# Optimization experiments

Hardware: AMD Instinct MI355X
Metric: run time of the kernel (lower is better)

Reference implementation:

```python
import jax, jax.numpy as jnp
import numpy as np

B, T, S = 64, 128, 16
E = 512           # d2v input size
H = 512           # bi-LSTM output size (args.d2v_embed)
Hh = H // 2       # per-direction hidden
NL = 2            # num_layers
ED = 128          # args.embedding_dim
USERS, ARTS, PAD = 100000, 100000, 0


def setup_inputs() -> dict:
    key = jax.random.key(0)
    ks = jax.random.split(key, 32)
    p = 0.02
    inp = {}
    inp["x1"] = jax.random.normal(ks[0], (B, T, E), jnp.float32)
    inp["sample_d2v_embeds"] = jax.random.normal(ks[1], (B, T, S, H), jnp.float32)
    # LSTM params: layer-0 input E == layer-1 input H, so stackable. gate order i,f,g,o
    inp["lstm_Wih"] = jax.random.normal(ks[2], (NL, 2, 4 * Hh, E), jnp.float32) * p
    inp["lstm_Whh"] = jax.random.normal(ks[3], (NL, 2, 4 * Hh, Hh), jnp.float32) * p
    inp["lstm_bih"] = jax.random.normal(ks[4], (NL, 2, 4 * Hh), jnp.float32) * p
    inp["lstm_bhh"] = jax.random.normal(ks[5], (NL, 2, 4 * Hh), jnp.float32) * p
    inp["attn_W1"] = jax.random.normal(ks[6], (H, H), jnp.float32) * p
    inp["attn_b1"] = jax.random.normal(ks[7], (H,), jnp.float32) * p
    inp["attn_w2"] = jax.random.normal(ks[8], (H,), jnp.float32) * p
    inp["rnn_mlp_W"] = jax.random.normal(ks[9], (64, H), jnp.float32) * p
    inp["rnn_mlp_b"] = jax.random.normal(ks[10], (64,), jnp.float32) * p
    inp["user_table"] = jax.random.normal(ks[11], (USERS, ED), jnp.float32) * p
    inp["art_table"] = (jax.random.normal(ks[12], (ARTS, ED), jnp.float32) * p).at[PAD].set(0.0)
    inp["em_W1"] = jax.random.normal(ks[13], (128, ED), jnp.float32) * p
    inp["em_b1"] = jax.random.normal(ks[14], (128,), jnp.float32) * p
    inp["em_W2"] = jax.random.normal(ks[15], (64, 128), jnp.float32) * p
    inp["em_b2"] = jax.random.normal(ks[16], (64,), jnp.float32) * p
    inp["lm_W1"] = jax.random.normal(ks[17], (256, 128), jnp.float32) * p
    inp["lm_b1"] = jax.random.normal(ks[18], (256,), jnp.float32) * p
    inp["lm_W2"] = jax.random.normal(ks[19], (128, 256), jnp.float32) * p
    inp["lm_b2"] = jax.random.normal(ks[20], (128,), jnp.float32) * p
    inp["lm_W3"] = jax.random.normal(ks[21], (64, 128), jnp.float32) * p
    inp["lm_b3"] = jax.random.normal(ks[22], (64,), jnp.float32) * p
    inp["lm_W4"] = jax.random.normal(ks[23], (1, 64), jnp.float32) * p
    inp["lm_b4"] = jax.random.normal(ks[24], (1,), jnp.float32) * p
    inp["x2"] = 0  # unused '_' arg
    inp["cate"] = jax.random.randint(ks[25], (B, T), 0, 10)  # unused by forward
    lens = jax.random.randint(ks[26], (B,), 1, T + 1)
    inp["seq_lens"] = jnp.sort(lens)[::-1]  # pack requires descending
    inp["user_ids"] = jax.random.randint(ks[27], (B,), 0, USERS)
    inp["sample_ids"] = jax.random.randint(ks[28], (B, T, S), 0, ARTS)
    return inp


def _bilstm(x, lens, Wih, Whh, bih, bhh):
    # Packed bidirectional LSTM == padded LSTM with state updates masked to t < len.
    Bc, Tc, _ = x.shape
    tmask = jnp.arange(Tc)[None, :] < lens[:, None]       # [B,T]
    m_t = tmask.T[:, :, None]                             # [T,B,1]
    for l in range(NL):
        outs = []
        for d, rev in ((0, False), (1, True)):
            xg = jnp.einsum('bti,gi->tbg', x, Wih[l, d]) + bih[l, d]  # [T,B,4Hh]
            Whh_ld, bhh_ld = Whh[l, d], bhh[l, d]

            def step(carry, inp_t, Whh_ld=Whh_ld, bhh_ld=bhh_ld):
                h, c = carry
                xg_t, m = inp_t
                g = xg_t + h @ Whh_ld.T + bhh_ld
                i_, f_, g_, o_ = jnp.split(g, 4, axis=-1)
                c2 = jax.nn.sigmoid(f_) * c + jax.nn.sigmoid(i_) * jnp.tanh(g_)
                h2 = jax.nn.sigmoid(o_) * jnp.tanh(c2)
                h = jnp.where(m, h2, h)
                c = jnp.where(m, c2, c)
                return (h, c), h

            init = (jnp.zeros((Bc, Hh), x.dtype), jnp.zeros((Bc, Hh), x.dtype))
            _, hs = jax.lax.scan(step, init, (xg, m_t), reverse=rev)
            outs.append(jnp.transpose(hs, (1, 0, 2)))
        x = jnp.concatenate(outs, axis=-1)                # [B,T,H]
    return x, tmask


def reference(x1, sample_d2v_embeds, lstm_Wih, lstm_Whh, lstm_bih, lstm_bhh,
              attn_W1, attn_b1, attn_w2, rnn_mlp_W, rnn_mlp_b,
              user_table, art_table, em_W1, em_b1, em_W2, em_b2,
              lm_W1, lm_b1, lm_W2, lm_b2, lm_W3, lm_b3, lm_W4, lm_b4,
              x2, cate, seq_lens, user_ids, sample_ids):
    rnn, tmask = _bilstm(x1, seq_lens, lstm_Wih, lstm_Whh, lstm_bih, lstm_bhh)
    # per-key MLP attention score, causal softmax, weighted sum (the packed double loop)
    sc = jnp.einsum('bth,h->bt', jnp.tanh(jnp.einsum('bth,oh->bto', rnn, attn_W1) + attn_b1), attn_w2)
    causal = jnp.tril(jnp.ones((rnn.shape[1], rnn.shape[1]), bool))
    logits = jnp.where(causal[None, :, :], sc[:, None, :], jnp.float32(-1e30))
    a = jax.nn.softmax(logits, axis=-1)                   # [B,T(query),T(key)]
    ctx = jnp.einsum('bts,bsh->bth', a, rnn)
    ctx = jnp.where(tmask[:, :, None], ctx, 0.0)          # rnn_step zeros at padded t
    # embedding branch
    ue = user_table[user_ids]                             # [B,ED]
    se = art_table[sample_ids]                            # [B,T,S,ED]
    e = ue[:, None, None, :] * se
    e = jax.nn.relu(e @ em_W1.T + em_b1)
    e = jax.nn.relu(e @ em_W2.T + em_b2)                  # [B,T,S,64]
    # rnn branch
    r = ctx[:, :, None, :] * sample_d2v_embeds
    r = r @ rnn_mlp_W.T + rnn_mlp_b                       # [B,T,S,64]
    z = jnp.concatenate([e, r], axis=-1)                  # [B,T,S,128]
    z = jax.nn.relu(z @ lm_W1.T + lm_b1)
    z = jax.nn.relu(z @ lm_W2.T + lm_b2)
    z = jax.nn.relu(z @ lm_W3.T + lm_b3)
    z = jax.nn.sigmoid(z @ lm_W4.T + lm_b4)
    return jnp.squeeze(z, axis=-1)                        # [B,T,S]
```

## Files before the change

kernel.cpp:

```cpp
#include <hip/hip_runtime.h>
#include <cstddef>

namespace {

constexpr int T = 128;

typedef unsigned short u16;
typedef unsigned int u32;
typedef __attribute__((ext_vector_type(8))) short short8;
typedef __attribute__((ext_vector_type(4))) float f32x4;
typedef __attribute__((ext_vector_type(4))) int i32x4;

__device__ __forceinline__ u16 f2bf(float x) {
  u32 u = __float_as_uint(x);
  u = (u + 0x7FFFu + ((u >> 16) & 1u)) >> 16;
  return (u16)u;
}
__device__ __forceinline__ float bf2f(u16 v) {
  return __uint_as_float(((u32)v) << 16);
}
__device__ __forceinline__ float sigf(float x) {
  return __builtin_amdgcn_rcpf(1.f + __builtin_amdgcn_exp2f(-1.44269504f * x));
}
__device__ __forceinline__ float tanh2(float x) {
  return 1.f - 2.f * __builtin_amdgcn_rcpf(1.f + __builtin_amdgcn_exp2f(2.88539008f * x));
}
__device__ __forceinline__ void bar_lds() {
  asm volatile("s_waitcnt lgkmcnt(0)\n\ts_barrier" ::: "memory");
}

constexpr int O_WIH = 0;
constexpr int O_AW1 = 2097152;
constexpr int O_EM1 = 2359296;
constexpr int O_EM2 = 2375680;
constexpr int O_MLP = 2383872;
constexpr int O_LW1 = 2416640;
constexpr int O_LW2 = 2449408;
constexpr int O_LW3 = 2482176;
constexpr int N_WBF = 2490368;

__global__ __launch_bounds__(256)
void k_prep(const float* __restrict__ wih, const float* __restrict__ aw1,
            const float* __restrict__ e1, const float* __restrict__ e2,
            const float* __restrict__ mw, const float* __restrict__ l1,
            const float* __restrict__ l2, const float* __restrict__ l3,
            u16* __restrict__ wbf) {
  int i = blockIdx.x * 256 + threadIdx.x;
  if (i >= N_WBF) return;
  float v;
  if (i < O_AW1)      v = wih[i];
  else if (i < O_EM1) v = aw1[i - O_AW1];
  else if (i < O_EM2) v = e1[i - O_EM1];
  else if (i < O_MLP) v = e2[i - O_EM2];
  else if (i < O_LW1) v = mw[i - O_MLP];
  else if (i < O_LW2) v = l1[i - O_LW1];
  else if (i < O_LW3) v = l2[i - O_LW2];
  else                v = l3[i - O_LW3];
  wbf[i] = f2bf(v);
}

__global__ __launch_bounds__(256)
void k_prepw(const float* __restrict__ whh, signed char* __restrict__ wq) {
  int i = blockIdx.x * 256 + threadIdx.x;
  float v = whh[i] * 1016.f;
  v = fminf(fmaxf(v, -127.f), 127.f);
  wq[i] = (signed char)(int)rintf(v);
}

__global__ __launch_bounds__(256)
void k_xg_mfma(const float* __restrict__ X, const u16* __restrict__ Wbf,
               const float* __restrict__ bi, const float* __restrict__ bh,
               float* __restrict__ xg) {
  __shared__ __align__(16) u16 sx[32 * 520];
  int tid = threadIdx.x;
  int rowbase = blockIdx.x * 32;
  int nchunk = blockIdx.y;
  for (int idx = tid; idx < 4096; idx += 256) {
    int r = idx >> 7, k4 = idx & 127;
    float4 v = *(const float4*)(X + (size_t)(rowbase + r) * 512 + k4 * 4);
    u32* p = (u32*)(sx + r * 520 + k4 * 4);
    p[0] = (u32)f2bf(v.x) | ((u32)f2bf(v.y) << 16);
    p[1] = (u32)f2bf(v.z) | ((u32)f2bf(v.w) << 16);
  }
  __syncthreads();
  int w = tid >> 6, lane = tid & 63;
  int msub = w >> 1, nhalf = w & 1;
  int mbase = msub * 16;
  int nb0 = nchunk * 256 + nhalf * 128;
  f32x4 acc[8];
#pragma unroll
  for (int i = 0; i < 8; ++i) acc[i] = f32x4{0.f, 0.f, 0.f, 0.f};
  for (int kt = 0; kt < 16; ++kt) {
    short8 a = *(const short8*)(sx + (mbase + (lane & 15)) * 520 + kt * 32 + (lane >> 4) * 8);
#pragma unroll
    for (int nt = 0; nt < 8; ++nt) {
      short8 b = *(const short8*)(Wbf + (size_t)(nb0 + nt * 16 + (lane & 15)) * 512 +
                                  kt * 32 + (lane >> 4) * 8);
      acc[nt] = __builtin_amdgcn_mfma_f32_16x16x32_bf16(a, b, acc[nt], 0, 0, 0);
    }
  }
  int mr = mbase + (lane >> 4) * 4;
#pragma unroll
  for (int nt = 0; nt < 8; ++nt) {
    int n = nb0 + nt * 16 + (lane & 15);
    float bb = bi[n] + bh[n];
#pragma unroll
    for (int r = 0; r < 4; ++r)
      xg[(size_t)(rowbase + mr + r) * 2048 + n] = acc[nt][r] + bb;
  }
}

__global__ __launch_bounds__(512, 1)
void k_lstm6(const float* __restrict__ xg, const signed char* __restrict__ wq,
             const int* __restrict__ lens, float* __restrict__ out, int layer) {
  __shared__ __align__(16) signed char hq[2][16 * 272];
  const int d = blockIdx.x >> 2, bg = blockIdx.x & 3;
  const int tid = threadIdx.x;
  const int jc = tid >> 6, l = tid & 63, ln = l & 15, lk = l >> 4;
  const int mb = bg * 16;

  i32x4 Bq[4][2][4];
  const signed char* wbase = wq + (size_t)(layer * 2 + d) * 262144;
#pragma unroll
  for (int g = 0; g < 4; ++g)
#pragma unroll
    for (int js = 0; js < 2; ++js)
#pragma unroll
      for (int kc = 0; kc < 4; ++kc) {
        int n = g * 256 + jc * 32 + js * 16 + ln;
        Bq[g][js][kc] = *(const i32x4*)(wbase + (size_t)n * 256 + kc * 64 + lk * 16);
      }

  int mlen[4];
#pragma unroll
  for (int r = 0; r < 4; ++r) mlen[r] = lens[mb + lk * 4 + r];

  float cst[2][4], hst[2][4];
#pragma unroll
  for (int js = 0; js < 2; ++js)
#pragma unroll
    for (int r = 0; r < 4; ++r) { cst[js][r] = 0.f; hst[js][r] = 0.f; }

  const float DEQ = 1.f / (1016.f * 127.f);

  for (int s = 0; s < 128; ++s) {
    const int t = d ? (127 - s) : s;

    float xv[4][2][4];
#pragma unroll
    for (int g = 0; g < 4; ++g)
#pragma unroll
      for (int js = 0; js < 2; ++js)
#pragma unroll
        for (int r = 0; r < 4; ++r)
          xv[g][js][r] = xg[((size_t)(mb + lk * 4 + r) * 128 + t) * 2048 +
                            d * 1024 + g * 256 + jc * 32 + js * 16 + ln];

    i32x4 acc[4][2];
#pragma unroll
    for (int g = 0; g < 4; ++g)
#pragma unroll
      for (int js = 0; js < 2; ++js) acc[g][js] = i32x4{0, 0, 0, 0};

    if (s > 0) {
      const signed char* hr = hq[(s & 1) ^ 1];
#pragma unroll
      for (int kc = 0; kc < 4; ++kc) {
        i32x4 a = *(const i32x4*)(hr + ln * 272 + kc * 64 + lk * 16);
#pragma unroll
        for (int g = 0; g < 4; ++g)
#pragma unroll
          for (int js = 0; js < 2; ++js)
            acc[g][js] = __builtin_amdgcn_mfma_i32_16x16x64_i8(a, Bq[g][js][kc],
                                                               acc[g][js], 0, 0, 0);
      }
    }

    signed char* hw = hq[s & 1];
#pragma unroll
    for (int js = 0; js < 2; ++js)
#pragma unroll
      for (int r = 0; r < 4; ++r) {
        float gi = (float)acc[0][js][r] * DEQ + xv[0][js][r];
        float gf = (float)acc[1][js][r] * DEQ + xv[1][js][r];
        float gg = (float)acc[2][js][r] * DEQ + xv[2][js][r];
        float go = (float)acc[3][js][r] * DEQ + xv[3][js][r];
        float c2 = sigf(gf) * cst[js][r] + sigf(gi) * tanh2(gg);
        float h2 = sigf(go) * tanh2(c2);
        const int m = lk * 4 + r;
        bool upd = t < mlen[r];
        cst[js][r] = upd ? c2 : cst[js][r];
        float hn = upd ? h2 : hst[js][r];
        hst[js][r] = hn;
        const int j = jc * 32 + js * 16 + ln;
        out[((size_t)(mb + m) * 128 + t) * 512 + d * 256 + j] = hn;
        hw[m * 272 + j] = (signed char)(int)rintf(hn * 127.f);
      }
    bar_lds();
  }
}

__global__ __launch_bounds__(256)
void k_attn(const float* __restrict__ rnn, const u16* __restrict__ W1bf,
            const float* __restrict__ b1, const float* __restrict__ w2,
            float* __restrict__ sc) {
  __shared__ __align__(16) u16 sx[32 * 520];
  __shared__ float sred[32];
  int tid = threadIdx.x;
  int rowbase = blockIdx.x * 32;
  for (int idx = tid; idx < 4096; idx += 256) {
    int r = idx >> 7, k4 = idx & 127;
    float4 v = *(const float4*)(rnn + (size_t)(rowbase + r) * 512 + k4 * 4);
    u32* p = (u32*)(sx + r * 520 + k4 * 4);
    p[0] = (u32)f2bf(v.x) | ((u32)f2bf(v.y) << 16);
    p[1] = (u32)f2bf(v.z) | ((u32)f2bf(v.w) << 16);
  }
  if (tid < 32) sred[tid] = 0.f;
  __syncthreads();
  int w = tid >> 6, lane = tid & 63;
  int msub = w >> 1, nhalf = w & 1;
  int mbase = msub * 16;
  float psum[4] = {0.f, 0.f, 0.f, 0.f};
  for (int ng = 0; ng < 4; ++ng) {
    f32x4 acc[4];
#pragma unroll
    for (int i = 0; i < 4; ++i) acc[i] = f32x4{0.f, 0.f, 0.f, 0.f};
    for (int kt = 0; kt < 16; ++kt) {
      short8 a = *(const short8*)(sx + (mbase + (lane & 15)) * 520 + kt * 32 + (lane >> 4) * 8);
#pragma unroll
      for (int nt = 0; nt < 4; ++nt) {
        int nrow = nhalf * 256 + ng * 64 + nt * 16 + (lane & 15);
        short8 b = *(const short8*)(W1bf + (size_t)nrow * 512 + kt * 32 + (lane >> 4) * 8);
        acc[nt] = __builtin_amdgcn_mfma_f32_16x16x32_bf16(a, b, acc[nt], 0, 0, 0);
      }
    }
#pragma unroll
    for (int nt = 0; nt < 4; ++nt) {
      int n = nhalf * 256 + ng * 64 + nt * 16 + (lane & 15);
      float wn = w2[n], bn = b1[n];
#pragma unroll
      for (int r = 0; r < 4; ++r) psum[r] += wn * tanh2(acc[nt][r] + bn);
    }
  }
#pragma unroll
  for (int off = 8; off >= 1; off >>= 1)
#pragma unroll
    for (int r = 0; r < 4; ++r) psum[r] += __shfl_xor(psum[r], off);
  if ((lane & 15) == 0) {
#pragma unroll
    for (int r = 0; r < 4; ++r)
      atomicAdd(&sred[msub * 16 + (lane >> 4) * 4 + r], psum[r]);
  }
  __syncthreads();
  if (tid < 32) sc[rowbase + tid] = sred[tid];
}

__global__ __launch_bounds__(128)
void k_ctx(const float* __restrict__ sc, const float* __restrict__ rnn,
           const int* __restrict__ lens, float* __restrict__ ctx) {
  int b = blockIdx.x;
  int h = blockIdx.y * 128 + threadIdx.x;
  __shared__ float ex[T];
  ex[threadIdx.x] = expf(sc[b * T + threadIdx.x]);
  __syncthreads();
  int len = lens[b];
  float acc = 0.f, den = 0.f;
  for (int t = 0; t < T; ++t) {
    float wv = ex[t];
    den += wv;
    acc += wv * rnn[((size_t)b * T + t) * 512 + h];
    ctx[((size_t)b * T + t) * 512 + h] = (t < len) ? (acc / den) : 0.f;
  }
}

template <int NT, int KT, bool RELU>
__device__ __forceinline__ void stage_mfma(const u16* __restrict__ Wbf,
                                           const float* __restrict__ bias,
                                           const u16* A, int lda,
                                           u16* O, int ldo, int nofs,
                                           int lane, int msub, int nhalf) {
  f32x4 acc[NT];
#pragma unroll
  for (int i = 0; i < NT; ++i) acc[i] = f32x4{0.f, 0.f, 0.f, 0.f};
  int mbase = msub * 16;
  int nb0 = nhalf * (NT * 16);
#pragma unroll
  for (int kt = 0; kt < KT; ++kt) {
    short8 a = *(const short8*)(A + (mbase + (lane & 15)) * lda + kt * 32 + (lane >> 4) * 8);
#pragma unroll
    for (int nt = 0; nt < NT; ++nt) {
      short8 b = *(const short8*)(Wbf + (size_t)(nb0 + nt * 16 + (lane & 15)) * (KT * 32) +
                                  kt * 32 + (lane >> 4) * 8);
      acc[nt] = __builtin_amdgcn_mfma_f32_16x16x32_bf16(a, b, acc[nt], 0, 0, 0);
    }
  }
  int mr = mbase + (lane >> 4) * 4;
#pragma unroll
  for (int nt = 0; nt < NT; ++nt) {
    int nl = nb0 + nt * 16 + (lane & 15);
    float bv = bias[nl];
#pragma unroll
    for (int r = 0; r < 4; ++r) {
      float v = acc[nt][r] + bv;
      if (RELU) v = fmaxf(v, 0.f);
      O[(mr + r) * ldo + nofs + nl] = f2bf(v);
    }
  }
}

__global__ __launch_bounds__(256)
void k_sample(const float* __restrict__ ctx, const float* __restrict__ d2v,
              const float* __restrict__ user_table, const float* __restrict__ art_table,
              const int* __restrict__ user_ids, const int* __restrict__ sample_ids,
              const u16* __restrict__ wbf,
              const float* __restrict__ em_b1, const float* __restrict__ em_b2,
              const float* __restrict__ mlp_b,
              const float* __restrict__ lm_b1, const float* __restrict__ lm_b2,
              const float* __restrict__ lm_b3,
              const float* __restrict__ lm_W4, const float* __restrict__ lm_b4,
              float* __restrict__ out) {
  __shared__ __align__(16) u16 bufA[32 * 264];
  __shared__ __align__(16) u16 bufB[32 * 264];
  __shared__ __align__(16) u16 bufC[32 * 136];
  __shared__ float sred[32];
  int tid = threadIdx.x, lane = tid & 63, w = tid >> 6;
  int msub = w >> 1, nhalf = w & 1;
  int mbase = msub * 16;
  int rowbase = blockIdx.x * 32;

  if (tid < 32) sred[tid] = 0.f;

  for (int idx = tid; idx < 1024; idx += 256) {
    int r = idx >> 5, k4 = idx & 31;
    int m = rowbase + r;
    int sid = sample_ids[m];
    int uid = user_ids[m >> 11];
    float4 u = *(const float4*)(user_table + (size_t)uid * 128 + k4 * 4);
    float4 a = *(const float4*)(art_table + (size_t)sid * 128 + k4 * 4);
    u32* p = (u32*)(bufA + r * 264 + k4 * 4);
    p[0] = (u32)f2bf(u.x * a.x) | ((u32)f2bf(u.y * a.y) << 16);
    p[1] = (u32)f2bf(u.z * a.z) | ((u32)f2bf(u.w * a.w) << 16);
  }
  bar_lds();
  stage_mfma<4, 4, true>(wbf + O_EM1, em_b1, bufA, 264, bufB, 264, 0, lane, msub, nhalf);
  bar_lds();
  stage_mfma<2, 4, true>(wbf + O_EM2, em_b2, bufB, 264, bufC, 136, 0, lane, msub, nhalf);
  for (int idx = tid; idx < 2048; idx += 256) {
    int r = idx >> 6, k4 = idx & 63;
    int m = rowbase + r;
    int bt = m >> 4;
    float4 cx = *(const float4*)(ctx + (size_t)bt * 512 + k4 * 4);
    float4 dv = *(const float4*)(d2v + (size_t)m * 512 + k4 * 4);
    u32* p = (u32*)(bufA + r * 264 + k4 * 4);
    p[0] = (u32)f2bf(cx.x * dv.x) | ((u32)f2bf(cx.y * dv.y) << 16);
    p[1] = (u32)f2bf(cx.z * dv.z) | ((u32)f2bf(cx.w * dv.w) << 16);
  }
  bar_lds();

  f32x4 racc[2];
  racc[0] = f32x4{0.f, 0.f, 0.f, 0.f};
  racc[1] = f32x4{0.f, 0.f, 0.f, 0.f};
  for (int kc = 0; kc < 2; ++kc) {
#pragma unroll
    for (int kt = 0; kt < 8; ++kt) {
      short8 a = *(const short8*)(bufA + (mbase + (lane & 15)) * 264 + kt * 32 + (lane >> 4) * 8);
#pragma unroll
      for (int nt = 0; nt < 2; ++nt) {
        int n = nhalf * 32 + nt * 16 + (lane & 15);
        short8 b = *(const short8*)(wbf + O_MLP + (size_t)n * 512 + kc * 256 +
                                    kt * 32 + (lane >> 4) * 8);
        racc[nt] = __builtin_amdgcn_mfma_f32_16x16x32_bf16(a, b, racc[nt], 0, 0, 0);
      }
    }
    bar_lds();
    if (kc == 0) {
      for (int idx = tid; idx < 2048; idx += 256) {
        int r = idx >> 6, k4 = idx & 63;
        int m = rowbase + r;
        int bt = m >> 4;
        float4 cx = *(const float4*)(ctx + (size_t)bt * 512 + 256 + k4 * 4);
        float4 dv = *(const float4*)(d2v + (size_t)m * 512 + 256 + k4 * 4);
        u32* p = (u32*)(bufA + r * 264 + k4 * 4);
        p[0] = (u32)f2bf(cx.x * dv.x) | ((u32)f2bf(cx.y * dv.y) << 16);
        p[1] = (u32)f2bf(cx.z * dv.z) | ((u32)f2bf(cx.w * dv.w) << 16);
      }
      bar_lds();
    }
  }
  {
    int mr = mbase + (lane >> 4) * 4;
#pragma unroll
    for (int nt = 0; nt < 2; ++nt) {
      int nl = nhalf * 32 + nt * 16 + (lane & 15);
      float bv = mlp_b[nl];
#pragma unroll
      for (int r = 0; r < 4; ++r)
        bufC[(mr + r) * 136 + 64 + nl] = f2bf(racc[nt][r] + bv);
    }
  }
  bar_lds();
  stage_mfma<8, 4, true>(wbf + O_LW1, lm_b1, bufC, 136, bufB, 264, 0, lane, msub, nhalf);
  bar_lds();
  stage_mfma<4, 8, true>(wbf + O_LW2, lm_b2, bufB, 264, bufA, 264, 0, lane, msub, nhalf);
  bar_lds();

  {
    f32x4 acc[2];
    acc[0] = f32x4{0.f, 0.f, 0.f, 0.f};
    acc[1] = f32x4{0.f, 0.f, 0.f, 0.f};
#pragma unroll
    for (int kt = 0; kt < 4; ++kt) {
      short8 a = *(const short8*)(bufA + (mbase + (lane & 15)) * 264 + kt * 32 + (lane >> 4) * 8);
#pragma unroll
      for (int nt = 0; nt < 2; ++nt) {
        int n = nhalf * 32 + nt * 16 + (lane & 15);
        short8 b = *(const short8*)(wbf + O_LW3 + (size_t)n * 128 +
                                    kt * 32 + (lane >> 4) * 8);
        acc[nt] = __builtin_amdgcn_mfma_f32_16x16x32_bf16(a, b, acc[nt], 0, 0, 0);
      }
    }
    float psum[4] = {0.f, 0.f, 0.f, 0.f};
#pragma unroll
    for (int nt = 0; nt < 2; ++nt) {
      int nl = nhalf * 32 + nt * 16 + (lane & 15);
      float bv = lm_b3[nl], w4 = lm_W4[nl];
#pragma unroll
      for (int r = 0; r < 4; ++r) psum[r] += w4 * fmaxf(acc[nt][r] + bv, 0.f);
    }
#pragma unroll
    for (int off = 8; off >= 1; off >>= 1)
#pragma unroll
      for (int r = 0; r < 4; ++r) psum[r] += __shfl_xor(psum[r], off);
    if ((lane & 15) == 0) {
#pragma unroll
      for (int r = 0; r < 4; ++r)
        atomicAdd(&sred[mbase + (lane >> 4) * 4 + r], psum[r]);
    }
  }
  bar_lds();
  if (tid < 32) out[rowbase + tid] = sigf(sred[tid] + lm_b4[0]);
}

}

extern "C" void kernel_launch(void* const* d_in, const int* in_sizes, int n_in,
                              void* d_out, int out_size, void* d_ws, size_t ws_size,
                              hipStream_t stream) {
  const float* x1   = (const float*)d_in[0];
  const float* d2v  = (const float*)d_in[1];
  const float* Wih  = (const float*)d_in[2];
  const float* Whh  = (const float*)d_in[3];
  const float* bih  = (const float*)d_in[4];
  const float* bhh  = (const float*)d_in[5];
  const float* aW1  = (const float*)d_in[6];
  const float* ab1  = (const float*)d_in[7];
  const float* aw2  = (const float*)d_in[8];
  const float* mlpW = (const float*)d_in[9];
  const float* mlpb = (const float*)d_in[10];
  const float* utab = (const float*)d_in[11];
  const float* atab = (const float*)d_in[12];
  const float* emW1 = (const float*)d_in[13];
  const float* emb1 = (const float*)d_in[14];
  const float* emW2 = (const float*)d_in[15];
  const float* emb2 = (const float*)d_in[16];
  const float* lmW1 = (const float*)d_in[17];
  const float* lmb1 = (const float*)d_in[18];
  const float* lmW2 = (const float*)d_in[19];
  const float* lmb2 = (const float*)d_in[20];
  const float* lmW3 = (const float*)d_in[21];
  const float* lmb3 = (const float*)d_in[22];
  const float* lmW4 = (const float*)d_in[23];
  const float* lmb4 = (const float*)d_in[24];
  const int* lens   = (const int*)d_in[27];
  const int* uids   = (const int*)d_in[28];
  const int* sids   = (const int*)d_in[29];
  float* out = (float*)d_out;

  float* ws = (float*)d_ws;
  signed char* WQ = (signed char*)ws;
  float* SC  = ws + 262144;
  u16* WBF = (u16*)(ws + 270336);
  float* XG  = ws + 1515520;
  float* R0  = ws + 18292736;
  float* R1  = ws + 22487040;
  float* CTX = ws + 18292736;

  k_prep<<<(N_WBF + 255) / 256, 256, 0, stream>>>(Wih, aW1, emW1, emW2, mlpW,
                                                  lmW1, lmW2, lmW3, WBF);
  k_prepw<<<4096, 256, 0, stream>>>(Whh, WQ);
  k_xg_mfma<<<dim3(256, 8), 256, 0, stream>>>(x1, WBF + O_WIH, bih, bhh, XG);
  k_lstm6<<<8, 512, 0, stream>>>(XG, WQ, lens, R0, 0);
  k_xg_mfma<<<dim3(256, 8), 256, 0, stream>>>(R0, WBF + O_WIH + 1048576,
                                              bih + 2048, bhh + 2048, XG);
  k_lstm6<<<8, 512, 0, stream>>>(XG, WQ, lens, R1, 1);
  k_attn<<<256, 256, 0, stream>>>(R1, WBF + O_AW1, ab1, aw2, SC);
  k_ctx<<<dim3(64, 4), 128, 0, stream>>>(SC, R1, lens, CTX);
  k_sample<<<4096, 256, 0, stream>>>(CTX, d2v, utab, atab, uids, sids, WBF,
                                     emb1, emb2, mlpb, lmb1, lmb2, lmb3,
                                     lmW4, lmb4, out);
}
```

Before: 1.260 ms.

## Prefetch next-step LSTM input gates and hoist d2v loads in final MLP kernel

In the recurrent LSTM kernel, the precomputed input-gate values for step s+1 are loaded into registers during step s, so global load latency overlaps the MFMA recurrence instead of sitting on the serial critical path. In the final MLP kernel, the embedding gathers and both halves of the d2v tile are issued into registers early, before the earlier MFMA stages, to overlap memory latency with compute. Both changes raise register pressure substantially (extra 32 floats per thread in LSTM, 16 float4 in MLP), which may reduce occupancy or cause spills.

```diff
diff --git a/kernel.cpp b/kernel.cpp
--- a/kernel.cpp
+++ b/kernel.cpp
@@ -143,18 +143,34 @@
 
   const float DEQ = 1.f / (1016.f * 127.f);
 
+  float xv[4][2][4];
+  {
+    int t0 = d ? 127 : 0;
+#pragma unroll
+    for (int g = 0; g < 4; ++g)
+#pragma unroll
+      for (int js = 0; js < 2; ++js)
+#pragma unroll
+        for (int r = 0; r < 4; ++r)
+          xv[g][js][r] = xg[((size_t)(mb + lk * 4 + r) * 128 + t0) * 2048 +
+                            d * 1024 + g * 256 + jc * 32 + js * 16 + ln];
+  }
+
   for (int s = 0; s < 128; ++s) {
     const int t = d ? (127 - s) : s;
 
-    float xv[4][2][4];
-#pragma unroll
-    for (int g = 0; g < 4; ++g)
-#pragma unroll
-      for (int js = 0; js < 2; ++js)
-#pragma unroll
-        for (int r = 0; r < 4; ++r)
-          xv[g][js][r] = xg[((size_t)(mb + lk * 4 + r) * 128 + t) * 2048 +
-                            d * 1024 + g * 256 + jc * 32 + js * 16 + ln];
+    float xvn[4][2][4];
+    if (s < 127) {
+      const int tn = d ? (127 - (s + 1)) : (s + 1);
+#pragma unroll
+      for (int g = 0; g < 4; ++g)
+#pragma unroll
+        for (int js = 0; js < 2; ++js)
+#pragma unroll
+          for (int r = 0; r < 4; ++r)
+            xvn[g][js][r] = xg[((size_t)(mb + lk * 4 + r) * 128 + tn) * 2048 +
+                               d * 1024 + g * 256 + jc * 32 + js * 16 + ln];
+    }
 
     i32x4 acc[4][2];
 #pragma unroll
@@ -196,6 +212,15 @@
         out[((size_t)(mb + m) * 128 + t) * 512 + d * 256 + j] = hn;
         hw[m * 272 + j] = (signed char)(int)rintf(hn * 127.f);
       }
+
+    if (s < 127) {
+#pragma unroll
+      for (int g = 0; g < 4; ++g)
+#pragma unroll
+        for (int js = 0; js < 2; ++js)
+#pragma unroll
+          for (int r = 0; r < 4; ++r) xv[g][js][r] = xvn[g][js][r];
+    }
     bar_lds();
   }
 }
@@ -330,13 +355,31 @@
 
   if (tid < 32) sred[tid] = 0.f;
 
-  for (int idx = tid; idx < 1024; idx += 256) {
+  float4 uu[4], aa[4];
+#pragma unroll
+  for (int it = 0; it < 4; ++it) {
+    int idx = it * 256 + tid;
     int r = idx >> 5, k4 = idx & 31;
     int m = rowbase + r;
     int sid = sample_ids[m];
     int uid = user_ids[m >> 11];
-    float4 u = *(const float4*)(user_table + (size_t)uid * 128 + k4 * 4);
-    float4 a = *(const float4*)(art_table + (size_t)sid * 128 + k4 * 4);
+    uu[it] = *(const float4*)(user_table + (size_t)uid * 128 + k4 * 4);
+    aa[it] = *(const float4*)(art_table + (size_t)sid * 128 + k4 * 4);
+  }
+  float4 dd0[8];
+#pragma unroll
+  for (int it = 0; it < 8; ++it) {
+    int idx = it * 256 + tid;
+    int r = idx >> 6, k4 = idx & 63;
+    int m = rowbase + r;
+    dd0[it] = *(const float4*)(d2v + (size_t)m * 512 + k4 * 4);
+  }
+
+#pragma unroll
+  for (int it = 0; it < 4; ++it) {
+    int idx = it * 256 + tid;
+    int r = idx >> 5, k4 = idx & 31;
+    float4 u = uu[it], a = aa[it];
     u32* p = (u32*)(bufA + r * 264 + k4 * 4);
     p[0] = (u32)f2bf(u.x * a.x) | ((u32)f2bf(u.y * a.y) << 16);
     p[1] = (u32)f2bf(u.z * a.z) | ((u32)f2bf(u.w * a.w) << 16);
@@ -345,12 +388,22 @@
   stage_mfma<4, 4, true>(wbf + O_EM1, em_b1, bufA, 264, bufB, 264, 0, lane, msub, nhalf);
   bar_lds();
   stage_mfma<2, 4, true>(wbf + O_EM2, em_b2, bufB, 264, bufC, 136, 0, lane, msub, nhalf);
-  for (int idx = tid; idx < 2048; idx += 256) {
+  float4 dd1[8];
+#pragma unroll
+  for (int it = 0; it < 8; ++it) {
+    int idx = it * 256 + tid;
+    int r = idx >> 6, k4 = idx & 63;
+    int m = rowbase + r;
+    dd1[it] = *(const float4*)(d2v + (size_t)m * 512 + 256 + k4 * 4);
+  }
+#pragma unroll
+  for (int it = 0; it < 8; ++it) {
+    int idx = it * 256 + tid;
     int r = idx >> 6, k4 = idx & 63;
     int m = rowbase + r;
     int bt = m >> 4;
     float4 cx = *(const float4*)(ctx + (size_t)bt * 512 + k4 * 4);
-    float4 dv = *(const float4*)(d2v + (size_t)m * 512 + k4 * 4);
+    float4 dv = dd0[it];
     u32* p = (u32*)(bufA + r * 264 + k4 * 4);
     p[0] = (u32)f2bf(cx.x * dv.x) | ((u32)f2bf(cx.y * dv.y) << 16);
     p[1] = (u32)f2bf(cx.z * dv.z) | ((u32)f2bf(cx.w * dv.w) << 16);
@@ -374,12 +427,14 @@
     }
     bar_lds();
     if (kc == 0) {
-      for (int idx = tid; idx < 2048; idx += 256) {
+#pragma unroll
+      for (int it = 0; it < 8; ++it) {
+        int idx = it * 256 + tid;
         int r = idx >> 6, k4 = idx & 63;
         int m = rowbase + r;
         int bt = m >> 4;
         float4 cx = *(const float4*)(ctx + (size_t)bt * 512 + 256 + k4 * 4);
-        float4 dv = *(const float4*)(d2v + (size_t)m * 512 + 256 + k4 * 4);
+        float4 dv = dd1[it];
         u32* p = (u32*)(bufA + r * 264 + k4 * 4);
         p[0] = (u32)f2bf(cx.x * dv.x) | ((u32)f2bf(cx.y * dv.y) << 16);
         p[1] = (u32)f2bf(cx.z * dv.z) | ((u32)f2bf(cx.w * dv.w) << 16);
```

Result: slower. 1.378 ms (+9.4%).
